# Kernel optimization log

Measured on AMD Instinct MI355X. Metric: run time of the kernel, lower is better.

The kernel has to match this reference:

```python
import jax, jax.numpy as jnp
import numpy as np

H, KVH, P = 32, 8, 64          # heads, kv heads, head_dim (state dim n == P here)
GROUPS = H // KVH
D = H * P                      # hidden = 2048
CONV_DIM = (H + 2 * KVH) * P   # 3072
PROJ = (H + 2 * KVH + H) * P + H  # 5152
CHUNK = 128
EPS = 1e-5
B_, L_ = 2, 2048


def silu(x):
    return x * jax.nn.sigmoid(x)


def segsum(x):
    # x: [..., T] -> [..., T, T] with out[i, j] = sum_{j < k <= i} x[k], -inf above diag
    T = x.shape[-1]
    xb = jnp.broadcast_to(x[..., :, None], x.shape + (T,))
    strict = jnp.tril(jnp.ones((T, T), bool), -1)
    s = jnp.cumsum(jnp.where(strict, xb, 0.0), axis=-2)
    incl = jnp.tril(jnp.ones((T, T), bool))
    return jnp.where(incl, s, -jnp.inf)


def ssd(x, A, Bm, Cm, chunk):
    # Mamba2 chunked scan (SSD). x:[b,l,h,p] (already * dt), A:[b,l,h] (A*dt), B/C:[b,l,h,n]
    b, l, h, p = x.shape
    n = Bm.shape[-1]
    c = l // chunk
    x = x.reshape(b, c, chunk, h, p)
    Bm = Bm.reshape(b, c, chunk, h, n)
    Cm = Cm.reshape(b, c, chunk, h, n)
    A = A.reshape(b, c, chunk, h).transpose(0, 3, 1, 2)  # [b,h,c,l]
    Acs = jnp.cumsum(A, axis=-1)
    # intra-chunk (diagonal blocks)
    Lmat = jnp.exp(segsum(A))  # [b,h,c,l,l]
    Yd = jnp.einsum('bclhn,bcshn,bhcls,bcshp->bclhp', Cm, Bm, Lmat, x)
    # chunk-final states
    dstates = jnp.exp(Acs[..., -1:] - Acs)  # [b,h,c,l]
    states = jnp.einsum('bclhn,bhcl,bclhp->bchpn', Bm, dstates, x)
    states = jnp.concatenate([jnp.zeros_like(states[:, :1]), states], axis=1)
    dchunk = jnp.exp(segsum(jnp.pad(Acs[..., -1], ((0, 0), (0, 0), (1, 0)))))  # [b,h,c+1,c+1]
    states = jnp.einsum('bhzc,bchpn->bzhpn', dchunk, states)[:, :-1]
    # inter-chunk contribution
    Yo = jnp.einsum('bclhn,bchpn,bhcl->bclhp', Cm, states, jnp.exp(Acs))
    return (Yd + Yo).reshape(b, l, h, p)


def setup_inputs() -> dict:
    key = jax.random.key(0)
    ks = jax.random.split(key, 8)
    s = 0.02
    hidden_states = jax.random.normal(ks[0], (B_, L_, D), jnp.float32)
    W_vkqgdt = jax.random.normal(ks[1], (PROJ, D), jnp.float32) * s
    # conv init: identity tap on last position + small noise so grads are nontrivial
    conv_w = jnp.zeros((CONV_DIM, 2), jnp.float32).at[:, 1].set(1.0)
    conv_w = conv_w + jax.random.normal(ks[2], (CONV_DIM, 2), jnp.float32) * s
    conv_b = jax.random.normal(ks[3], (CONV_DIM,), jnp.float32) * s
    # dt_bias init as in the module: inverse-softplus of dt ~ LogUniform(1e-3, 1e-1)
    u = jax.random.uniform(ks[4], (H,), jnp.float32)
    dtv = jnp.exp(u * (np.log(0.1) - np.log(0.001)) + np.log(0.001))
    dtv = jnp.clip(dtv, 0.001)
    dt_bias = dtv + jnp.log(-jnp.expm1(-dtv))
    A_log_bias = jnp.zeros((H,), jnp.float32)
    gnorm_w = jnp.ones((P,), jnp.float32)
    W_o = jax.random.normal(ks[5], (D, D), jnp.float32) * s
    return {'hidden_states': hidden_states, 'W_vkqgdt': W_vkqgdt, 'conv_w': conv_w,
            'conv_b': conv_b, 'dt_bias': dt_bias, 'A_log_bias': A_log_bias,
            'gnorm_w': gnorm_w, 'W_o': W_o}


def reference(hidden_states, W_vkqgdt, conv_w, conv_b, dt_bias, A_log_bias, gnorm_w, W_o):
    b, l, _ = hidden_states.shape
    proj = hidden_states @ W_vkqgdt.T  # [b,l,PROJ]
    vkq, g, dt = jnp.split(proj, [CONV_DIM, CONV_DIM + H * P], axis=2)
    # causal depthwise conv (kernel=2) + SiLU
    x_prev = jnp.pad(vkq, ((0, 0), (1, 0), (0, 0)))[:, :-1]
    vkq = silu(x_prev * conv_w[:, 0] + vkq * conv_w[:, 1] + conv_b)
    v, k, q = jnp.split(vkq, [KVH * P, 2 * KVH * P], axis=2)
    v = jnp.repeat(v.reshape(b, l, KVH, P), GROUPS, axis=2)  # [b,l,H,P]
    k = jnp.repeat(k.reshape(b, l, KVH, P), GROUPS, axis=2)
    q = q.reshape(b, l, H, P)
    dt = jax.nn.softplus(dt + dt_bias)          # [b,l,H]
    A = -jnp.exp(A_log_bias.astype(jnp.float32))  # [H]
    y = ssd(v * dt[..., None], dt * A, k, q, CHUNK)  # x=v, B=k, C=q
    # fused RMSNorm + swish gate
    g = g.reshape(b, l, H, P)
    yn = y * jax.lax.rsqrt(jnp.mean(y * y, axis=-1, keepdims=True) + EPS) * gnorm_w
    y_true = (yn * silu(g)).reshape(b, l, D)
    return y_true @ W_o.T
```

## Files before the change

### kernel.cpp

```cpp
#include <hip/hip_runtime.h>
#include <hip/hip_bf16.h>
#include <math.h>

typedef __bf16 bf16;
typedef __bf16 bf16x4 __attribute__((ext_vector_type(4)));
typedef __bf16 bf16x8 __attribute__((ext_vector_type(8)));
typedef float f32x4 __attribute__((ext_vector_type(4)));

#define NB 2
#define LSEQ 2048
#define NH 32
#define NKVH 8
#define HD 64
#define DMODEL 2048
#define CONVD 3072
#define NPROJ 5152
#define NPADN 5248
#define NCHUNK 16
#define CHUNK 128
#define ROWS 4096
#define EPSF 1e-5f

__device__ __forceinline__ float fsilu(float x) { return x / (1.0f + __expf(-x)); }
__device__ __forceinline__ float fsoftplus(float raw) {
  return (raw > 20.0f) ? raw : log1pf(__expf(raw));
}

__device__ __forceinline__ void gld_lds16(const void* g, void* l) {
  __builtin_amdgcn_global_load_lds(
      (const __attribute__((address_space(1))) void*)g,
      (__attribute__((address_space(3))) void*)l, 16, 0, 0);
}

__device__ __forceinline__ int swz64(int row, int col) {
  return row * 64 + ((((col >> 3) ^ row) & 7) << 3) + (col & 7);
}
__device__ __forceinline__ int swz128(int row, int col) {
  return row * 128 + (((col >> 3) ^ (row & 7)) << 3) + (col & 7);
}

__device__ __forceinline__ void stage64(const bf16* gsrc, bf16* lds, int tid, int nelem) {
  for (int i0 = 0; i0 < nelem; i0 += 2048) {
    int e = i0 + tid * 8;
    int row = e >> 6;
    int sc = ((tid & 7) ^ (row & 7)) << 3;
    gld_lds16((const void*)(gsrc + (row << 6) + sc), (void*)(lds + e));
  }
}
__device__ __forceinline__ void stage128(const bf16* gsrc, bf16* lds, int tid, int nelem) {
  for (int i0 = 0; i0 < nelem; i0 += 2048) {
    int e = i0 + tid * 8;
    int row = e >> 7;
    int sc = (((tid & 15) ^ (row & 7))) << 3;
    gld_lds16((const void*)(gsrc + (row << 7) + sc), (void*)(lds + e));
  }
}

__device__ __forceinline__ void wave_scan128(float& a0, float& a1, int lane) {
#pragma unroll
  for (int off = 1; off < 64; off <<= 1) {
    float t0 = __shfl_up(a0, off);
    float t1 = __shfl_up(a1, off);
    if (lane >= off) { a0 += t0; a1 += t1; }
  }
  a1 += __shfl(a0, 63);
}

__global__ __launch_bounds__(256) void cast_all_kernel(
    const float* __restrict__ hs, const float* __restrict__ w1, const float* __restrict__ wo,
    bf16* __restrict__ hs_b, bf16* __restrict__ w1_b, bf16* __restrict__ wo_b) {
  const long n1 = (long)ROWS * DMODEL / 4;
  const long n2 = (long)NPADN * DMODEL / 4;
  const long n3 = (long)DMODEL * DMODEL / 4;
  long total = n1 + n2 + n3;
  long stride = (long)gridDim.x * blockDim.x;
  for (long i = blockIdx.x * (long)blockDim.x + threadIdx.x; i < total; i += stride) {
    if (i < n1) {
      float4 v = ((const float4*)hs)[i];
      ((bf16x4*)hs_b)[i] = bf16x4{(bf16)v.x, (bf16)v.y, (bf16)v.z, (bf16)v.w};
    } else if (i < n1 + n2) {
      long j = i - n1;
      int n = (int)((j * 4) >> 11);
      bf16x4 o = {};
      if (n < NPROJ) {
        float4 v = ((const float4*)w1)[j];
        o = bf16x4{(bf16)v.x, (bf16)v.y, (bf16)v.z, (bf16)v.w};
      }
      ((bf16x4*)w1_b)[j] = o;
    } else {
      long j = i - n1 - n2;
      float4 v = ((const float4*)wo)[j];
      ((bf16x4*)wo_b)[j] = bf16x4{(bf16)v.x, (bf16)v.y, (bf16)v.z, (bf16)v.w};
    }
  }
}

template <typename OutT>
__global__ __launch_bounds__(256) void gemm_bt_kernel(
    const bf16* __restrict__ A, const bf16* __restrict__ B, OutT* __restrict__ C,
    int M, int N, int K, int ntx) {
  __shared__ __align__(16) bf16 As[128 * 64];
  __shared__ __align__(16) bf16 Bs[128 * 64];
  const int tid = threadIdx.x;
  const int lane = tid & 63;
  const int wave = tid >> 6;
  const int wm = wave >> 1, wn = wave & 1;

  const int GM = 8;
  int lid = blockIdx.x;
  int group = GM * ntx;
  int gid = lid / group;
  int rem = lid - gid * group;
  int bm = gid * GM + (rem % GM);
  int bn = rem / GM;

  f32x4 acc[4][4] = {};

  const bf16* Ab = A + (long)bm * 128 * K;
  const bf16* Bb = B + (long)bn * 128 * K;

  const int colsw = (((lane & 7) ^ ((lane >> 3) & 7)) << 3);
  const int fbA = (wm * 64 + (lane & 15)) * 64 + ((((lane >> 4) ^ (lane & 7))) << 3);
  const int fbB = (wn * 64 + (lane & 15)) * 64 + ((((lane >> 4) ^ (lane & 7))) << 3);

  for (int k0 = 0; k0 < K; k0 += 64) {
#pragma unroll
    for (int j = 0; j < 4; ++j) {
      int q = wave * 4 + j;
      int e = q * 512 + lane * 8;
      int row = q * 8 + (lane >> 3);
      gld_lds16((const void*)(Ab + (long)row * K + k0 + colsw), (void*)(As + e));
      gld_lds16((const void*)(Bb + (long)row * K + k0 + colsw), (void*)(Bs + e));
    }
    __syncthreads();
#pragma unroll
    for (int ks2 = 0; ks2 < 2; ++ks2) {
      bf16x8 af[4], bfb[4];
#pragma unroll
      for (int mi = 0; mi < 4; ++mi)
        af[mi] = *(const bf16x8*)(As + ((fbA + mi * 1024) ^ (ks2 << 5)));
#pragma unroll
      for (int ni = 0; ni < 4; ++ni)
        bfb[ni] = *(const bf16x8*)(Bs + ((fbB + ni * 1024) ^ (ks2 << 5)));
#pragma unroll
      for (int mi = 0; mi < 4; ++mi)
#pragma unroll
        for (int ni = 0; ni < 4; ++ni)
          acc[mi][ni] = __builtin_amdgcn_mfma_f32_16x16x32_bf16(af[mi], bfb[ni], acc[mi][ni], 0, 0, 0);
    }
    __syncthreads();
  }

#pragma unroll
  for (int mi = 0; mi < 4; ++mi) {
    int rbase = bm * 128 + wm * 64 + mi * 16 + (lane >> 4) * 4;
#pragma unroll
    for (int ni = 0; ni < 4; ++ni) {
      int col = bn * 128 + wn * 64 + ni * 16 + (lane & 15);
#pragma unroll
      for (int r = 0; r < 4; ++r)
        C[(long)(rbase + r) * N + col] = (OutT)acc[mi][ni][r];
    }
  }
}

__global__ __launch_bounds__(256) void prep_kernel(
    const bf16* __restrict__ proj, const float* __restrict__ conv_w,
    const float* __restrict__ conv_b, const float* __restrict__ dt_bias,
    const float* __restrict__ A_log,
    bf16* __restrict__ Qc, bf16* __restrict__ Kc, bf16* __restrict__ Kt,
    bf16* __restrict__ Vt, float* __restrict__ dtb, float* __restrict__ adtb) {
  __shared__ float tile[128][65];
  int blk = blockIdx.x, tid = threadIdx.x;

  if (blk < 1024) {
    int h = blk & 31, c = (blk >> 5) & 15, b = blk >> 9;
    long rowbase = (long)b * LSEQ + c * CHUNK;
    int j = tid >> 1, p0 = (tid & 1) * 32;
    const bf16* cur = proj + (rowbase + j) * NPADN;
    bool hp = (c > 0) || (j > 0);
    int chb = 1024 + h * 64;
    bf16* outb = Qc + (long)blk * 8192 + j * 64;
#pragma unroll
    for (int pp = 0; pp < 32; pp += 4) {
      int p = p0 + pp, ch = chb + p;
      bf16x4 cu = *(const bf16x4*)(cur + ch);
      bf16x4 pv = {};
      if (hp) pv = *(const bf16x4*)(cur + ch - NPADN);
      float4 wa = *(const float4*)(conv_w + 2 * ch);
      float4 wb = *(const float4*)(conv_w + 2 * ch + 4);
      float4 bb = *(const float4*)(conv_b + ch);
      bf16x4 o;
      o[0] = (bf16)fsilu((float)pv[0] * wa.x + (float)cu[0] * wa.y + bb.x);
      o[1] = (bf16)fsilu((float)pv[1] * wa.z + (float)cu[1] * wa.w + bb.y);
      o[2] = (bf16)fsilu((float)pv[2] * wb.x + (float)cu[2] * wb.y + bb.z);
      o[3] = (bf16)fsilu((float)pv[3] * wb.z + (float)cu[3] * wb.w + bb.w);
      *(bf16x4*)(outb + p) = o;
    }
  } else if (blk < 1536) {
    int r = blk - 1024;
    bool isK = r < 256;
    int rr = isK ? r : r - 256;
    int kvh = rr & 7, c = (rr >> 3) & 15, b = rr >> 7;
    long rowbase = (long)b * LSEQ + c * CHUNK;
    int chb = (isK ? 512 : 0) + kvh * 64;
    int j = tid >> 1, p0 = (tid & 1) * 32;
    const bf16* cur = proj + (rowbase + j) * NPADN;
    bool hp = (c > 0) || (j > 0);
#pragma unroll
    for (int pp = 0; pp < 32; pp += 4) {
      int p = p0 + pp, ch = chb + p;
      bf16x4 cu = *(const bf16x4*)(cur + ch);
      bf16x4 pv = {};
      if (hp) pv = *(const bf16x4*)(cur + ch - NPADN);
      float4 wa = *(const float4*)(conv_w + 2 * ch);
      float4 wb = *(const float4*)(conv_w + 2 * ch + 4);
      float4 bb = *(const float4*)(conv_b + ch);
      tile[j][p + 0] = fsilu((float)pv[0] * wa.x + (float)cu[0] * wa.y + bb.x);
      tile[j][p + 1] = fsilu((float)pv[1] * wa.z + (float)cu[1] * wa.w + bb.y);
      tile[j][p + 2] = fsilu((float)pv[2] * wb.x + (float)cu[2] * wb.y + bb.z);
      tile[j][p + 3] = fsilu((float)pv[3] * wb.z + (float)cu[3] * wb.w + bb.w);
    }
    __syncthreads();
    long tb = (long)rr * 8192;
    if (isK) {
#pragma unroll
      for (int it = 0; it < 8; ++it) {
        int e = it * 1024 + tid * 4;
        int jj = e >> 6, n = e & 63;
        bf16x4 o = {(bf16)tile[jj][n], (bf16)tile[jj][n + 1], (bf16)tile[jj][n + 2], (bf16)tile[jj][n + 3]};
        *(bf16x4*)(Kc + tb + e) = o;
      }
#pragma unroll
      for (int it = 0; it < 8; ++it) {
        int e = it * 1024 + tid * 4;
        int n = e >> 7, jj = e & 127;
        bf16x4 o = {(bf16)tile[jj][n], (bf16)tile[jj + 1][n], (bf16)tile[jj + 2][n], (bf16)tile[jj + 3][n]};
        *(bf16x4*)(Kt + tb + e) = o;
      }
    } else {
#pragma unroll
      for (int it = 0; it < 8; ++it) {
        int e = it * 1024 + tid * 4;
        int n = e >> 7, jj = e & 127;
        bf16x4 o = {(bf16)tile[jj][n], (bf16)tile[jj + 1][n], (bf16)tile[jj + 2][n], (bf16)tile[jj + 3][n]};
        *(bf16x4*)(Vt + tb + e) = o;
      }
    }
  } else {
    int r = blk - 1536;
    int c = r & 15, b = r >> 4;
    long rowbase = (long)b * LSEQ + c * CHUNK;
    int j = tid >> 1, h0 = (tid & 1) * 16;
    const bf16* dr = proj + (rowbase + j) * NPADN + (CONVD + DMODEL);
    int obase = (b * 16 + c) * 32;
#pragma unroll
    for (int u = 0; u < 16; ++u) {
      int h = h0 + u;
      float raw = (float)dr[h] + dt_bias[h];
      float dtv = fsoftplus(raw);
      dtb[(long)(obase + h) * 128 + j] = dtv;
      adtb[(long)(obase + h) * 128 + j] = -__expf(A_log[h]) * dtv;
    }
  }
}

__global__ __launch_bounds__(256) void ssd_states_kernel(
    const bf16* __restrict__ Kt, const bf16* __restrict__ Vt,
    const float* __restrict__ dtb, const float* __restrict__ adtb,
    float* __restrict__ states, float* __restrict__ asum) {
  __shared__ __align__(16) bf16 Vs[64 * 128];
  __shared__ __align__(16) bf16 Ks[64 * 128];
  __shared__ float w[CHUNK];
  int bid = blockIdx.x;
  int h = bid & 31, c = (bid >> 5) & 15, b = bid >> 9;
  int kvh = h >> 2;
  int tid = threadIdx.x;
  int lane = tid & 63, wave = tid >> 6;
  long kvb = (long)(((b * 16 + c) * 8) + kvh) * 8192;

  stage128(Vt + kvb, Vs, tid, 8192);
  stage128(Kt + kvb, Ks, tid, 8192);

  float a0 = adtb[(long)bid * 128 + lane];
  float a1 = adtb[(long)bid * 128 + 64 + lane];
  float d0 = dtb[(long)bid * 128 + lane];
  float d1 = dtb[(long)bid * 128 + 64 + lane];
  wave_scan128(a0, a1, lane);
  float atot = __shfl(a1, 63);
  if (wave == 0) {
    w[lane] = d0 * __expf(atot - a0);
    w[64 + lane] = d1 * __expf(atot - a1);
  }
  __syncthreads();

#pragma unroll
  for (int it = 0; it < 4; ++it) {
    int e = it * 2048 + tid * 8;
    int row = e >> 7;
    int j0 = (((tid & 15) ^ (row & 7))) << 3;
    f32x4 wa = *(const f32x4*)(w + j0);
    f32x4 wb = *(const f32x4*)(w + j0 + 4);
    bf16x8 kv = *(const bf16x8*)(Ks + e);
    kv[0] = (bf16)((float)kv[0] * wa[0]); kv[1] = (bf16)((float)kv[1] * wa[1]);
    kv[2] = (bf16)((float)kv[2] * wa[2]); kv[3] = (bf16)((float)kv[3] * wa[3]);
    kv[4] = (bf16)((float)kv[4] * wb[0]); kv[5] = (bf16)((float)kv[5] * wb[1]);
    kv[6] = (bf16)((float)kv[6] * wb[2]); kv[7] = (bf16)((float)kv[7] * wb[3]);
    *(bf16x8*)(Ks + e) = kv;
  }
  __syncthreads();

  f32x4 sacc[4] = {};
#pragma unroll
  for (int ks = 0; ks < CHUNK; ks += 32) {
    bf16x8 af = *(const bf16x8*)(Vs + swz128(wave * 16 + (lane & 15), ks + (lane >> 4) * 8));
    bf16x8 bf_[4];
#pragma unroll
    for (int ni = 0; ni < 4; ++ni)
      bf_[ni] = *(const bf16x8*)(Ks + swz128(ni * 16 + (lane & 15), ks + (lane >> 4) * 8));
#pragma unroll
    for (int ni = 0; ni < 4; ++ni)
      sacc[ni] = __builtin_amdgcn_mfma_f32_16x16x32_bf16(af, bf_[ni], sacc[ni], 0, 0, 0);
  }
  float* sout = states + (long)bid * (HD * HD);
#pragma unroll
  for (int ni = 0; ni < 4; ++ni) {
    int n = ni * 16 + (lane & 15);
#pragma unroll
    for (int r = 0; r < 4; ++r) {
      int p = wave * 16 + (lane >> 4) * 4 + r;
      sout[p * HD + n] = sacc[ni][r];
    }
  }
  if (tid == 0) asum[(b * NH + h) * NCHUNK + c] = atot;
}

__global__ __launch_bounds__(256) void ssd_scan_kernel(
    const float* __restrict__ states, const float* __restrict__ asum,
    bf16* __restrict__ sprevb) {
  int bid = blockIdx.x;
  int s = bid & 7, h = (bid >> 3) & 31, b = bid >> 8;
  int e0 = s * 512 + threadIdx.x;
  int e1 = e0 + 256;
  float S0 = 0.f, S1 = 0.f;
  const float* as = asum + (b * NH + h) * NCHUNK;
  for (int c = 0; c < NCHUNK; ++c) {
    long off = ((long)((b * NCHUNK + c) * NH + h)) * (HD * HD);
    float g = __expf(as[c]);
    sprevb[off + e0] = (bf16)S0;
    sprevb[off + e1] = (bf16)S1;
    S0 = S0 * g + states[off + e0];
    S1 = S1 * g + states[off + e1];
  }
}

__global__ __launch_bounds__(256) void ssd_out_kernel(
    const bf16* __restrict__ Qc, const bf16* __restrict__ Kc, const bf16* __restrict__ Vt,
    const bf16* __restrict__ sprevb, const float* __restrict__ dtb,
    const float* __restrict__ adtb, const bf16* __restrict__ proj,
    const float* __restrict__ gnw, bf16* __restrict__ yg) {
  __shared__ __align__(16) bf16 Qs[128 * 64];
  __shared__ __align__(16) bf16 KVs[128 * 64];
  __shared__ __align__(16) bf16 G[128 * 128];
  __shared__ __align__(16) bf16 Sps[64 * 64];
  __shared__ float acs[CHUNK];
  __shared__ float dts[CHUNK];
  __shared__ float part[CHUNK][2];
  __shared__ float rs_l[CHUNK];

  int bid = blockIdx.x;
  int h = bid & 31, c = (bid >> 5) & 15, b = bid >> 9;
  int kvh = h >> 2;
  int tid = threadIdx.x;
  int lane = tid & 63, wave = tid >> 6;
  int wm = wave >> 1, wn = wave & 1;
  long rowbase = (long)b * LSEQ + c * CHUNK;
  long kvb = (long)(((b * 16 + c) * 8) + kvh) * 8192;

  stage64(Qc + (long)bid * 8192, Qs, tid, 8192);
  stage64(Kc + kvb, KVs, tid, 8192);
  stage64(sprevb + (long)bid * 4096, Sps, tid, 4096);

  float a0 = adtb[(long)bid * 128 + lane];
  float a1 = adtb[(long)bid * 128 + 64 + lane];
  float d0 = dtb[(long)bid * 128 + lane];
  float d1 = dtb[(long)bid * 128 + 64 + lane];
  wave_scan128(a0, a1, lane);
  if (wave == 0) {
    acs[lane] = a0; acs[64 + lane] = a1;
    dts[lane] = d0; dts[64 + lane] = d1;
  }
  __syncthreads();

  {
    f32x4 gacc[4][4] = {};
#pragma unroll
    for (int ks = 0; ks < HD; ks += 32) {
      bf16x8 af[4], bf_[4];
#pragma unroll
      for (int mi = 0; mi < 4; ++mi)
        af[mi] = *(const bf16x8*)(Qs + swz64(wm * 64 + mi * 16 + (lane & 15), ks + (lane >> 4) * 8));
#pragma unroll
      for (int ni = 0; ni < 4; ++ni)
        bf_[ni] = *(const bf16x8*)(KVs + swz64(wn * 64 + ni * 16 + (lane & 15), ks + (lane >> 4) * 8));
#pragma unroll
      for (int mi = 0; mi < 4; ++mi)
#pragma unroll
        for (int ni = 0; ni < 4; ++ni)
          gacc[mi][ni] = __builtin_amdgcn_mfma_f32_16x16x32_bf16(af[mi], bf_[ni], gacc[mi][ni], 0, 0, 0);
    }
    float aj[4], dj[4];
#pragma unroll
    for (int ni = 0; ni < 4; ++ni) {
      int j = wn * 64 + ni * 16 + (lane & 15);
      aj[ni] = acs[j];
      dj[ni] = dts[j];
    }
#pragma unroll
    for (int mi = 0; mi < 4; ++mi) {
#pragma unroll
      for (int r = 0; r < 4; ++r) {
        int i = wm * 64 + mi * 16 + (lane >> 4) * 4 + r;
        float ai = acs[i];
#pragma unroll
        for (int ni = 0; ni < 4; ++ni) {
          int j = wn * 64 + ni * 16 + (lane & 15);
          float gv = (j <= i) ? gacc[mi][ni][r] * __expf(ai - aj[ni]) * dj[ni] : 0.f;
          G[swz128(i, j)] = (bf16)gv;
        }
      }
    }
  }
  __syncthreads();

  stage128(Vt + kvb, KVs, tid, 8192);
  __syncthreads();

  f32x4 yacc[4][2] = {};
  f32x4 oacc[4][2] = {};
#pragma unroll
  for (int ks = 0; ks < CHUNK; ks += 32) {
    bf16x8 af[4], bf_[2];
#pragma unroll
    for (int mi = 0; mi < 4; ++mi)
      af[mi] = *(const bf16x8*)(G + swz128(wm * 64 + mi * 16 + (lane & 15), ks + (lane >> 4) * 8));
#pragma unroll
    for (int ni = 0; ni < 2; ++ni)
      bf_[ni] = *(const bf16x8*)(KVs + swz128(wn * 32 + ni * 16 + (lane & 15), ks + (lane >> 4) * 8));
#pragma unroll
    for (int mi = 0; mi < 4; ++mi)
#pragma unroll
      for (int ni = 0; ni < 2; ++ni)
        yacc[mi][ni] = __builtin_amdgcn_mfma_f32_16x16x32_bf16(af[mi], bf_[ni], yacc[mi][ni], 0, 0, 0);
  }
#pragma unroll
  for (int ks = 0; ks < HD; ks += 32) {
    bf16x8 af[4], bf_[2];
#pragma unroll
    for (int mi = 0; mi < 4; ++mi)
      af[mi] = *(const bf16x8*)(Qs + swz64(wm * 64 + mi * 16 + (lane & 15), ks + (lane >> 4) * 8));
#pragma unroll
    for (int ni = 0; ni < 2; ++ni)
      bf_[ni] = *(const bf16x8*)(Sps + swz64(wn * 32 + ni * 16 + (lane & 15), ks + (lane >> 4) * 8));
#pragma unroll
    for (int mi = 0; mi < 4; ++mi)
#pragma unroll
      for (int ni = 0; ni < 2; ++ni)
        oacc[mi][ni] = __builtin_amdgcn_mfma_f32_16x16x32_bf16(af[mi], bf_[ni], oacc[mi][ni], 0, 0, 0);
  }

  float yv[4][2][4];
#pragma unroll
  for (int mi = 0; mi < 4; ++mi) {
#pragma unroll
    for (int r = 0; r < 4; ++r) {
      int i = wm * 64 + mi * 16 + (lane >> 4) * 4 + r;
      float ei = __expf(acs[i]);
      float s = 0.f;
#pragma unroll
      for (int ni = 0; ni < 2; ++ni) {
        float v = yacc[mi][ni][r] + ei * oacc[mi][ni][r];
        yv[mi][ni][r] = v;
        s += v * v;
      }
      s += __shfl_xor(s, 1, 64);
      s += __shfl_xor(s, 2, 64);
      s += __shfl_xor(s, 4, 64);
      s += __shfl_xor(s, 8, 64);
      if ((lane & 15) == 0) part[i][wn] = s;
    }
  }
  __syncthreads();

  for (int i0 = 0; i0 < 8192; i0 += 2048) {
    int e = i0 + tid * 8;
    int row = e >> 6;
    int sc = ((tid & 7) ^ (row & 7)) << 3;
    gld_lds16((const void*)(proj + (rowbase + row) * NPADN + CONVD + h * 64 + sc),
              (void*)(KVs + e));
  }
  if (tid < CHUNK) rs_l[tid] = rsqrtf((part[tid][0] + part[tid][1]) * (1.0f / HD) + EPSF);
  __syncthreads();

#pragma unroll
  for (int mi = 0; mi < 4; ++mi) {
#pragma unroll
    for (int r = 0; r < 4; ++r) {
      int i = wm * 64 + mi * 16 + (lane >> 4) * 4 + r;
      long row = rowbase + i;
      float rs = rs_l[i];
#pragma unroll
      for (int ni = 0; ni < 2; ++ni) {
        int p = wn * 32 + ni * 16 + (lane & 15);
        float gval = (float)KVs[swz64(i, p)];
        float val = yv[mi][ni][r] * rs * gnw[p] * fsilu(gval);
        yg[row * (long)DMODEL + h * HD + p] = (bf16)val;
      }
    }
  }
}

extern "C" void kernel_launch(void* const* d_in, const int* in_sizes, int n_in,
                              void* d_out, int out_size, void* d_ws, size_t ws_size,
                              hipStream_t stream) {
  const float* hs      = (const float*)d_in[0];
  const float* W1      = (const float*)d_in[1];
  const float* conv_w  = (const float*)d_in[2];
  const float* conv_b  = (const float*)d_in[3];
  const float* dt_bias = (const float*)d_in[4];
  const float* A_log   = (const float*)d_in[5];
  const float* gnw     = (const float*)d_in[6];
  const float* Wo      = (const float*)d_in[7];

  char* p = (char*)d_ws;
  bf16* hs_b   = (bf16*)p;  p += (long)ROWS * DMODEL * 2;
  bf16* w1_b   = (bf16*)p;  p += (long)NPADN * DMODEL * 2;
  bf16* wo_b   = (bf16*)p;  p += (long)DMODEL * DMODEL * 2;
  bf16* proj   = (bf16*)p;  p += (long)ROWS * NPADN * 2;
  bf16* Qc     = (bf16*)p;  p += (long)1024 * 8192 * 2;
  bf16* Kc     = (bf16*)p;  p += (long)256 * 8192 * 2;
  bf16* Kt     = (bf16*)p;  p += (long)256 * 8192 * 2;
  bf16* Vt     = (bf16*)p;  p += (long)256 * 8192 * 2;
  float* dtb   = (float*)p; p += (long)ROWS * NH * 4;
  float* adtb  = (float*)p; p += (long)ROWS * NH * 4;
  float* st    = (float*)p; p += (long)NB * NCHUNK * NH * HD * HD * 4;
  bf16* sprevb = (bf16*)p;  p += (long)NB * NCHUNK * NH * HD * HD * 2;
  float* asum  = (float*)p; p += (long)NB * NH * NCHUNK * 4;
  bf16* yg     = (bf16*)p;  p += (long)ROWS * DMODEL * 2;

  cast_all_kernel<<<4096, 256, 0, stream>>>(hs, W1, Wo, hs_b, w1_b, wo_b);

  gemm_bt_kernel<bf16><<<(ROWS / 128) * (NPADN / 128), 256, 0, stream>>>(
      hs_b, w1_b, proj, ROWS, NPADN, DMODEL, NPADN / 128);

  prep_kernel<<<1568, 256, 0, stream>>>(proj, conv_w, conv_b, dt_bias, A_log,
                                        Qc, Kc, Kt, Vt, dtb, adtb);

  ssd_states_kernel<<<NB * NCHUNK * NH, 256, 0, stream>>>(Kt, Vt, dtb, adtb, st, asum);
  ssd_scan_kernel<<<NB * NH * 8, 256, 0, stream>>>(st, asum, sprevb);
  ssd_out_kernel<<<NB * NCHUNK * NH, 256, 0, stream>>>(
      Qc, Kc, Vt, sprevb, dtb, adtb, proj, gnw, yg);

  gemm_bt_kernel<float><<<(ROWS / 128) * (DMODEL / 128), 256, 0, stream>>>(
      yg, wo_b, (float*)d_out, ROWS, DMODEL, DMODEL, DMODEL / 128);
}
```

Measured before the change: 385.8 us.

## Replace GEMM with 256x128-tile 8-wave kernel using multi-buffered LDS prefetch

Replaces the 128x128 single-buffered GEMM with a 512-thread, 256x128-tile kernel. It triple-buffers A and double-buffers B in LDS, prefetches two k-tiles ahead, and splits each k-step into two MFMA phases interleaved with staging, using explicit waitcnt, barriers and setprio. The goal is to hide global-load latency behind MFMA work and raise per-block arithmetic intensity for both projection GEMMs. In exchange it needs more LDS and registers per block, has fewer blocks (e.g. 16x16=256 for the output GEMM), and relies on fragile hand-tuned synchronization.

```diff
diff --git a/kernel.cpp b/kernel.cpp
--- a/kernel.cpp
+++ b/kernel.cpp
@@ -53,6 +53,16 @@
     int row = e >> 7;
     int sc = (((tid & 15) ^ (row & 7))) << 3;
     gld_lds16((const void*)(gsrc + (row << 7) + sc), (void*)(lds + e));
+  }
+}
+
+__device__ __forceinline__ void stage_unit(const bf16* g, bf16* l, int row0, int ldg, int tid) {
+#pragma unroll
+  for (int it = 0; it < 2; ++it) {
+    int e = it * 4096 + tid * 8;
+    int r = row0 + (e >> 6);
+    int sc = ((tid & 7) ^ (r & 7)) << 3;
+    gld_lds16((const void*)(g + (long)r * ldg + sc), (void*)(l + row0 * 64 + e));
   }
 }
 
@@ -96,15 +106,15 @@
 }
 
 template <typename OutT>
-__global__ __launch_bounds__(256) void gemm_bt_kernel(
+__global__ __launch_bounds__(512, 2) void gemm8_kernel(
     const bf16* __restrict__ A, const bf16* __restrict__ B, OutT* __restrict__ C,
     int M, int N, int K, int ntx) {
-  __shared__ __align__(16) bf16 As[128 * 64];
-  __shared__ __align__(16) bf16 Bs[128 * 64];
+  __shared__ __align__(16) bf16 As[3 * 256 * 64];
+  __shared__ __align__(16) bf16 Bs[2 * 128 * 64];
   const int tid = threadIdx.x;
   const int lane = tid & 63;
   const int wave = tid >> 6;
-  const int wm = wave >> 1, wn = wave & 1;
+  const int wm = wave >> 2, wn = wave & 3;
 
   const int GM = 8;
   int lid = blockIdx.x;
@@ -114,49 +124,95 @@
   int bm = gid * GM + (rem % GM);
   int bn = rem / GM;
 
-  f32x4 acc[4][4] = {};
-
-  const bf16* Ab = A + (long)bm * 128 * K;
-  const bf16* Bb = B + (long)bn * 128 * K;
-
-  const int colsw = (((lane & 7) ^ ((lane >> 3) & 7)) << 3);
-  const int fbA = (wm * 64 + (lane & 15)) * 64 + ((((lane >> 4) ^ (lane & 7))) << 3);
-  const int fbB = (wn * 64 + (lane & 15)) * 64 + ((((lane >> 4) ^ (lane & 7))) << 3);
-
-  for (int k0 = 0; k0 < K; k0 += 64) {
-#pragma unroll
-    for (int j = 0; j < 4; ++j) {
-      int q = wave * 4 + j;
-      int e = q * 512 + lane * 8;
-      int row = q * 8 + (lane >> 3);
-      gld_lds16((const void*)(Ab + (long)row * K + k0 + colsw), (void*)(As + e));
-      gld_lds16((const void*)(Bb + (long)row * K + k0 + colsw), (void*)(Bs + e));
-    }
-    __syncthreads();
-#pragma unroll
-    for (int ks2 = 0; ks2 < 2; ++ks2) {
-      bf16x8 af[4], bfb[4];
-#pragma unroll
-      for (int mi = 0; mi < 4; ++mi)
-        af[mi] = *(const bf16x8*)(As + ((fbA + mi * 1024) ^ (ks2 << 5)));
-#pragma unroll
-      for (int ni = 0; ni < 4; ++ni)
-        bfb[ni] = *(const bf16x8*)(Bs + ((fbB + ni * 1024) ^ (ks2 << 5)));
-#pragma unroll
-      for (int mi = 0; mi < 4; ++mi)
-#pragma unroll
-        for (int ni = 0; ni < 4; ++ni)
-          acc[mi][ni] = __builtin_amdgcn_mfma_f32_16x16x32_bf16(af[mi], bfb[ni], acc[mi][ni], 0, 0, 0);
-    }
-    __syncthreads();
-  }
-
-#pragma unroll
-  for (int mi = 0; mi < 4; ++mi) {
-    int rbase = bm * 128 + wm * 64 + mi * 16 + (lane >> 4) * 4;
-#pragma unroll
-    for (int ni = 0; ni < 4; ++ni) {
-      int col = bn * 128 + wn * 64 + ni * 16 + (lane & 15);
+  const bf16* Ag = A + (long)bm * 256 * K;
+  const bf16* Bg = B + (long)bn * 128 * K;
+  const int NT = K >> 6;
+
+  stage_unit(Ag, As, 0, K, tid);
+  stage_unit(Ag, As, 128, K, tid);
+  stage_unit(Bg, Bs, 0, K, tid);
+  stage_unit(Ag + 64, As + 16384, 0, K, tid);
+  stage_unit(Ag + 64, As + 16384, 128, K, tid);
+  stage_unit(Bg + 64, Bs + 8192, 0, K, tid);
+
+  const int fbA = (wm * 128 + (lane & 15)) * 64 + (((lane >> 4) ^ (lane & 7)) << 3);
+  const int fbB = (wn * 32 + (lane & 15)) * 64 + (((lane >> 4) ^ (lane & 7)) << 3);
+
+  f32x4 acc[8][2] = {};
+
+  asm volatile("s_waitcnt vmcnt(6)" ::: "memory");
+  __builtin_amdgcn_s_barrier();
+
+  int ab = 0;
+  for (int t = 0; t < NT; ++t) {
+    const bf16* At = As + ab * 16384;
+    const bf16* Bt = Bs + (t & 1) * 8192;
+    int ab2 = ab + 2; if (ab2 >= 3) ab2 -= 3;
+    const bool pf = (t + 2) < NT;
+    const bf16* Agn = Ag + (t + 2) * 64;
+    const bf16* Bgn = Bg + (t + 2) * 64;
+
+    bf16x8 a0[4][2], bb[2][2];
+#pragma unroll
+    for (int mi = 0; mi < 4; ++mi)
+#pragma unroll
+      for (int ks = 0; ks < 2; ++ks)
+        a0[mi][ks] = *(const bf16x8*)(At + ((fbA + mi * 1024) ^ (ks << 5)));
+#pragma unroll
+    for (int ni = 0; ni < 2; ++ni)
+#pragma unroll
+      for (int ks = 0; ks < 2; ++ks)
+        bb[ni][ks] = *(const bf16x8*)(Bt + ((fbB + ni * 1024) ^ (ks << 5)));
+    if (pf) stage_unit(Agn, As + ab2 * 16384, 0, K, tid);
+    __builtin_amdgcn_s_barrier();
+    asm volatile("s_waitcnt lgkmcnt(0)" ::: "memory");
+    __builtin_amdgcn_sched_barrier(0);
+    __builtin_amdgcn_s_setprio(1);
+#pragma unroll
+    for (int mi = 0; mi < 4; ++mi)
+#pragma unroll
+      for (int ni = 0; ni < 2; ++ni)
+#pragma unroll
+        for (int ks = 0; ks < 2; ++ks)
+          acc[mi][ni] = __builtin_amdgcn_mfma_f32_16x16x32_bf16(a0[mi][ks], bb[ni][ks], acc[mi][ni], 0, 0, 0);
+    __builtin_amdgcn_s_setprio(0);
+    __builtin_amdgcn_s_barrier();
+
+    bf16x8 a1[4][2];
+#pragma unroll
+    for (int mi = 0; mi < 4; ++mi)
+#pragma unroll
+      for (int ks = 0; ks < 2; ++ks)
+        a1[mi][ks] = *(const bf16x8*)(At + ((fbA + 4096 + mi * 1024) ^ (ks << 5)));
+    if (pf) {
+      stage_unit(Agn, As + ab2 * 16384, 128, K, tid);
+      stage_unit(Bgn, Bs + (t & 1) * 8192, 0, K, tid);
+    }
+    __builtin_amdgcn_s_barrier();
+    asm volatile("s_waitcnt lgkmcnt(0)" ::: "memory");
+    __builtin_amdgcn_sched_barrier(0);
+    __builtin_amdgcn_s_setprio(1);
+#pragma unroll
+    for (int mi = 0; mi < 4; ++mi)
+#pragma unroll
+      for (int ni = 0; ni < 2; ++ni)
+#pragma unroll
+        for (int ks = 0; ks < 2; ++ks)
+          acc[4 + mi][ni] = __builtin_amdgcn_mfma_f32_16x16x32_bf16(a1[mi][ks], bb[ni][ks], acc[4 + mi][ni], 0, 0, 0);
+    __builtin_amdgcn_s_setprio(0);
+    if (pf) asm volatile("s_waitcnt vmcnt(6)" ::: "memory");
+    else    asm volatile("s_waitcnt vmcnt(0)" ::: "memory");
+    __builtin_amdgcn_s_barrier();
+
+    ab = (ab + 1 == 3) ? 0 : ab + 1;
+  }
+
+#pragma unroll
+  for (int mi = 0; mi < 8; ++mi) {
+    int rbase = bm * 256 + wm * 128 + mi * 16 + (lane >> 4) * 4;
+#pragma unroll
+    for (int ni = 0; ni < 2; ++ni) {
+      int col = bn * 128 + wn * 32 + ni * 16 + (lane & 15);
 #pragma unroll
       for (int r = 0; r < 4; ++r)
         C[(long)(rbase + r) * N + col] = (OutT)acc[mi][ni][r];
@@ -550,7 +606,7 @@
 
   cast_all_kernel<<<4096, 256, 0, stream>>>(hs, W1, Wo, hs_b, w1_b, wo_b);
 
-  gemm_bt_kernel<bf16><<<(ROWS / 128) * (NPADN / 128), 256, 0, stream>>>(
+  gemm8_kernel<bf16><<<(ROWS / 256) * (NPADN / 128), 512, 0, stream>>>(
       hs_b, w1_b, proj, ROWS, NPADN, DMODEL, NPADN / 128);
 
   prep_kernel<<<1568, 256, 0, stream>>>(proj, conv_w, conv_b, dt_bias, A_log,
@@ -561,6 +617,6 @@
   ssd_out_kernel<<<NB * NCHUNK * NH, 256, 0, stream>>>(
       Qc, Kc, Vt, sprevb, dtb, adtb, proj, gnw, yg);
 
-  gemm_bt_kernel<float><<<(ROWS / 128) * (DMODEL / 128), 256, 0, stream>>>(
+  gemm8_kernel<float><<<(ROWS / 256) * (DMODEL / 128), 512, 0, stream>>>(
       yg, wo_b, (float*)d_out, ROWS, DMODEL, DMODEL, DMODEL / 128);
 }
```

Result: faster. 372.9 us (-3.3%).

## Double-buffer GEMM LDS tiles with prefetch, XCD-aware block remap, and priority scheduling

Applied to the files above, without the earlier changes.

Both projection GEMMs now use a double-buffered LDS pipeline. The next K-tile is issued via global_load_lds while the current tile feeds MFMA, which replaces the previous load, sync, compute, sync loop. Block IDs are remapped so consecutive logical tiles land on the same XCD, meant to improve L2 reuse. The LDS fragments are read with explicit ds_read_b128 and the MFMA block is wrapped in s_setprio. This doubles LDS use to 64KB per block, which may limit occupancy, and relies on hand-placed waitcnt and barriers being correct.

```diff
diff --git a/kernel.cpp b/kernel.cpp
--- a/kernel.cpp
+++ b/kernel.cpp
@@ -32,6 +32,14 @@
       (__attribute__((address_space(3))) void*)l, 16, 0, 0);
 }
 
+__device__ __forceinline__ bf16x8 lds_read_b128(const bf16* p) {
+  bf16x8 r;
+  unsigned off = (unsigned)(unsigned long)(__attribute__((address_space(3))) bf16*)p;
+  asm volatile("ds_read_b128 %0, %1" : "=v"(r) : "v"(off));
+  return r;
+}
+#define SBAR() asm volatile("s_barrier" ::: "memory")
+
 __device__ __forceinline__ int swz64(int row, int col) {
   return row * 64 + ((((col >> 3) ^ row) & 7) << 3) + (col & 7);
 }
@@ -53,6 +61,16 @@
     int row = e >> 7;
     int sc = (((tid & 15) ^ (row & 7))) << 3;
     gld_lds16((const void*)(gsrc + (row << 7) + sc), (void*)(lds + e));
+  }
+}
+
+__device__ __forceinline__ void stage_tileY(const bf16* g, bf16* l, int ldg, int tid) {
+#pragma unroll
+  for (int it = 0; it < 4; ++it) {
+    int e = it * 2048 + tid * 8;
+    int r = e >> 6;
+    int sc = ((tid & 7) ^ (r & 7)) << 3;
+    gld_lds16((const void*)(g + (long)r * ldg + sc), (void*)(l + e));
   }
 }
 
@@ -96,11 +114,11 @@
 }
 
 template <typename OutT>
-__global__ __launch_bounds__(256) void gemm_bt_kernel(
+__global__ __launch_bounds__(256, 2) void gemm2p_kernel(
     const bf16* __restrict__ A, const bf16* __restrict__ B, OutT* __restrict__ C,
     int M, int N, int K, int ntx) {
-  __shared__ __align__(16) bf16 As[128 * 64];
-  __shared__ __align__(16) bf16 Bs[128 * 64];
+  __shared__ __align__(16) bf16 As[2 * 128 * 64];
+  __shared__ __align__(16) bf16 Bs[2 * 128 * 64];
   const int tid = threadIdx.x;
   const int lane = tid & 63;
   const int wave = tid >> 6;
@@ -108,47 +126,64 @@
 
   const int GM = 8;
   int lid = blockIdx.x;
+  {
+    int nwg = gridDim.x;
+    int xcd = lid & 7;
+    int q = nwg >> 3, r = nwg & 7;
+    lid = (xcd < r ? xcd * (q + 1) : r * (q + 1) + (xcd - r) * q) + (lid >> 3);
+  }
   int group = GM * ntx;
   int gid = lid / group;
   int rem = lid - gid * group;
   int bm = gid * GM + (rem % GM);
   int bn = rem / GM;
 
+  const bf16* Ag = A + (long)bm * 128 * K;
+  const bf16* Bg = B + (long)bn * 128 * K;
+  const int NT = K >> 6;
+
+  const int fbA = (wm * 64 + (lane & 15)) * 64 + (((lane >> 4) ^ (lane & 7)) << 3);
+  const int fbB = (wn * 64 + (lane & 15)) * 64 + (((lane >> 4) ^ (lane & 7)) << 3);
+
   f32x4 acc[4][4] = {};
 
-  const bf16* Ab = A + (long)bm * 128 * K;
-  const bf16* Bb = B + (long)bn * 128 * K;
-
-  const int colsw = (((lane & 7) ^ ((lane >> 3) & 7)) << 3);
-  const int fbA = (wm * 64 + (lane & 15)) * 64 + ((((lane >> 4) ^ (lane & 7))) << 3);
-  const int fbB = (wn * 64 + (lane & 15)) * 64 + ((((lane >> 4) ^ (lane & 7))) << 3);
-
-  for (int k0 = 0; k0 < K; k0 += 64) {
-#pragma unroll
-    for (int j = 0; j < 4; ++j) {
-      int q = wave * 4 + j;
-      int e = q * 512 + lane * 8;
-      int row = q * 8 + (lane >> 3);
-      gld_lds16((const void*)(Ab + (long)row * K + k0 + colsw), (void*)(As + e));
-      gld_lds16((const void*)(Bb + (long)row * K + k0 + colsw), (void*)(Bs + e));
-    }
-    __syncthreads();
-#pragma unroll
-    for (int ks2 = 0; ks2 < 2; ++ks2) {
-      bf16x8 af[4], bfb[4];
-#pragma unroll
-      for (int mi = 0; mi < 4; ++mi)
-        af[mi] = *(const bf16x8*)(As + ((fbA + mi * 1024) ^ (ks2 << 5)));
+  stage_tileY(Ag, As, K, tid);
+  stage_tileY(Bg, Bs, K, tid);
+  asm volatile("s_waitcnt vmcnt(0)" ::: "memory");
+  SBAR();
+
+  for (int t = 0; t < NT; ++t) {
+    const int c = t & 1;
+    const bf16* At = As + c * 8192;
+    const bf16* Bt = Bs + c * 8192;
+    if (t + 1 < NT) {
+      stage_tileY(Ag + (t + 1) * 64, As + (c ^ 1) * 8192, K, tid);
+      stage_tileY(Bg + (t + 1) * 64, Bs + (c ^ 1) * 8192, K, tid);
+    }
+    bf16x8 af[4][2], bf_[4][2];
+#pragma unroll
+    for (int mi = 0; mi < 4; ++mi)
+#pragma unroll
+      for (int ks = 0; ks < 2; ++ks)
+        af[mi][ks] = lds_read_b128(At + ((fbA + mi * 1024) ^ (ks << 5)));
+#pragma unroll
+    for (int ni = 0; ni < 4; ++ni)
+#pragma unroll
+      for (int ks = 0; ks < 2; ++ks)
+        bf_[ni][ks] = lds_read_b128(Bt + ((fbB + ni * 1024) ^ (ks << 5)));
+    asm volatile("s_waitcnt lgkmcnt(0)" ::: "memory");
+    __builtin_amdgcn_sched_barrier(0);
+    __builtin_amdgcn_s_setprio(1);
+#pragma unroll
+    for (int mi = 0; mi < 4; ++mi)
 #pragma unroll
       for (int ni = 0; ni < 4; ++ni)
-        bfb[ni] = *(const bf16x8*)(Bs + ((fbB + ni * 1024) ^ (ks2 << 5)));
-#pragma unroll
-      for (int mi = 0; mi < 4; ++mi)
-#pragma unroll
-        for (int ni = 0; ni < 4; ++ni)
-          acc[mi][ni] = __builtin_amdgcn_mfma_f32_16x16x32_bf16(af[mi], bfb[ni], acc[mi][ni], 0, 0, 0);
-    }
-    __syncthreads();
+#pragma unroll
+        for (int ks = 0; ks < 2; ++ks)
+          acc[mi][ni] = __builtin_amdgcn_mfma_f32_16x16x32_bf16(af[mi][ks], bf_[ni][ks], acc[mi][ni], 0, 0, 0);
+    __builtin_amdgcn_s_setprio(0);
+    asm volatile("s_waitcnt vmcnt(0)" ::: "memory");
+    SBAR();
   }
 
 #pragma unroll
@@ -550,7 +585,7 @@
 
   cast_all_kernel<<<4096, 256, 0, stream>>>(hs, W1, Wo, hs_b, w1_b, wo_b);
 
-  gemm_bt_kernel<bf16><<<(ROWS / 128) * (NPADN / 128), 256, 0, stream>>>(
+  gemm2p_kernel<bf16><<<(ROWS / 128) * (NPADN / 128), 256, 0, stream>>>(
       hs_b, w1_b, proj, ROWS, NPADN, DMODEL, NPADN / 128);
 
   prep_kernel<<<1568, 256, 0, stream>>>(proj, conv_w, conv_b, dt_bias, A_log,
@@ -561,6 +596,6 @@
   ssd_out_kernel<<<NB * NCHUNK * NH, 256, 0, stream>>>(
       Qc, Kc, Vt, sprevb, dtb, adtb, proj, gnw, yg);
 
-  gemm_bt_kernel<float><<<(ROWS / 128) * (DMODEL / 128), 256, 0, stream>>>(
+  gemm2p_kernel<float><<<(ROWS / 128) * (DMODEL / 128), 256, 0, stream>>>(
       yg, wo_b, (float*)d_out, ROWS, DMODEL, DMODEL, DMODEL / 128);
 }
```

New measurement: 353.2 us. 8.5% less time.
